# Performance work log

Measured on AMD Instinct MI355X. Metric: run time of the kernel, lower is better.

## Reference

```python
import jax, jax.numpy as jnp
from jax import lax
import numpy as np

GAMMA = 0.05   # GaussianKernel gamma (partial(GaussianKernel, 0.05)); assumed default for conv2 as well
EPS = 1e-5     # BatchNorm eps
DN = ('NCHW', 'OIHW', 'NCHW')


def gaussian_conv(x, w, gamma):
    """KernelConv2d with RBF kernel: out[b,o,i,j] = exp(-gamma * ||patch - w[o]||^2).
    Uses ||x-w||^2 = ||x||^2 - 2 x.w + ||w||^2 to avoid materializing im2col patches."""
    cross = lax.conv_general_dilated(x, w, (1, 1), 'VALID', dimension_numbers=DN)
    ones = jnp.ones((1, x.shape[1]) + w.shape[2:], x.dtype)
    xsq = lax.conv_general_dilated(x * x, ones, (1, 1), 'VALID', dimension_numbers=DN)
    wsq = jnp.sum(w * w, axis=(1, 2, 3))[None, :, None, None]
    return jnp.exp(-gamma * (xsq - 2.0 * cross + wsq))


def max_pool2(x):
    return lax.reduce_window(x, -jnp.inf, lax.max, (1, 1, 2, 2), (1, 1, 2, 2), 'VALID')


def batchnorm(x, g, b, m, v):
    # eval-mode BN with running stats
    scale = (g / jnp.sqrt(v + EPS))[None, :, None, None]
    return (x - m[None, :, None, None]) * scale + b[None, :, None, None]


def setup_inputs() -> dict:
    key = jax.random.key(0)
    ks = jax.random.split(key, 8)
    B, C, H = 128, 3, 96
    fea1, fea2, k1, k2, lin1, ncls = 32, 64, 5, 5, 256, 10
    flat = fea2 * 21 * 21  # 96->92->46->42->21
    return {
        'x': jax.random.normal(ks[0], (B, C, H, H), jnp.float32),
        'w1': jax.random.normal(ks[1], (fea1, C, k1, k1), jnp.float32) * 0.05,
        'w2': jax.random.normal(ks[2], (fea2, fea1, k2, k2), jnp.float32) * 0.05,
        'bn1_g': jnp.ones((fea1,), jnp.float32),
        'bn1_b': jnp.zeros((fea1,), jnp.float32),
        'bn1_m': jnp.zeros((fea1,), jnp.float32),
        'bn1_v': jnp.ones((fea1,), jnp.float32),
        'bn2_g': jnp.ones((fea2,), jnp.float32),
        'bn2_b': jnp.zeros((fea2,), jnp.float32),
        'bn2_m': jnp.zeros((fea2,), jnp.float32),
        'bn2_v': jnp.ones((fea2,), jnp.float32),
        'fc1_w': jax.random.normal(ks[3], (lin1, flat), jnp.float32) * 0.02,
        'fc1_b': jnp.zeros((lin1,), jnp.float32),
        'fc2_w': jax.random.normal(ks[4], (ncls, lin1), jnp.float32) * 0.02,
        'fc2_b': jnp.zeros((ncls,), jnp.float32),
    }


def reference(x, w1, w2, bn1_g, bn1_b, bn1_m, bn1_v, bn2_g, bn2_b, bn2_m, bn2_v,
              fc1_w, fc1_b, fc2_w, fc2_b):
    h = jax.nn.relu(max_pool2(gaussian_conv(x, w1, GAMMA)))
    h = batchnorm(h, bn1_g, bn1_b, bn1_m, bn1_v)
    # eval mode: Dropout2d is identity
    h = jax.nn.relu(max_pool2(gaussian_conv(h, w2, GAMMA)))
    h = batchnorm(h, bn2_g, bn2_b, bn2_m, bn2_v)
    h = h.reshape(h.shape[0], -1)
    h = jax.nn.relu(h @ fc1_w.T + fc1_b)
    # eval mode: dropout is identity
    h = jax.nn.relu(h @ fc2_w.T + fc2_b)
    return jax.nn.log_softmax(h, axis=1)
```

## Files before the change

kernel.cpp:

```cpp
#include <hip/hip_runtime.h>
#include <math.h>

#define GAMMA 0.05f
#define EPSBN 1e-5f

#define B_   128
#define H0   96
#define O1   32
#define P1   46
#define O2   64
#define H2C  42
#define P2   21
#define FLAT (O2*P2*P2)
#define L1N  256
#define NCLS 10
#define XW   104

typedef __attribute__((ext_vector_type(8))) short bf16x8;
typedef __attribute__((ext_vector_type(4))) float f32x4;
typedef __attribute__((ext_vector_type(16))) float f32x16;

static __device__ __forceinline__ float bf2f(unsigned short h) {
    return __uint_as_float(((unsigned int)h) << 16);
}
static __device__ __forceinline__ unsigned short f2bf(float f) {
    unsigned int u = __float_as_uint(f);
    u = (u + 0x7FFFu + ((u >> 16) & 1u)) >> 16;
    return (unsigned short)u;
}

__global__ void k_wprep(const float* __restrict__ w1, const float* __restrict__ w2,
                        unsigned short* __restrict__ w2bf, unsigned short* __restrict__ w1p8,
                        float* __restrict__ wsq1, float* __restrict__ wsq2) {
    int pb = blockIdx.x;
    int tid = threadIdx.x;
    for (int i = pb * 256 + tid; i < 51200 + 7168; i += 64 * 256) {
        if (i < 51200) {
            int e = i & 7, o = (i >> 3) & 63, hi = (i >> 9) & 1, ks = (i >> 10) & 1, kp = i >> 11;
            int ch = ks * 16 + hi * 8 + e;
            w2bf[i] = f2bf(-2.f * w2[((size_t)o * 32 + ch) * 25 + kp]);
        } else {
            int j = i - 51200;
            int ch = j & 7, o = (j >> 3) & 31, t = j >> 8;
            float v = 0.f;
            if (t < 25) {
                if (ch < 3) v = -2.f * w1[(size_t)(o * 3 + ch) * 25 + t];
                else if (ch == 3) v = 1.f;
            }
            w1p8[j] = f2bf(v);
        }
    }
    if (pb == 0) {
        int lt = tid;
        if (lt < 32) {
            const float* p = w1 + lt * 75;
            float s = 0.f;
            for (int i = 0; i < 75; ++i) s += p[i] * p[i];
            wsq1[lt] = s;
        } else if (lt < 96) {
            const float* p = w2 + (size_t)(lt - 32) * 800;
            float s = 0.f;
            for (int i = 0; i < 800; ++i) s += p[i] * p[i];
            wsq2[lt - 32] = s;
        }
    }
}

__global__ __launch_bounds__(256) void k_conv1m(
    const float* __restrict__ x, const unsigned short* __restrict__ w1p8,
    const float* __restrict__ wsq1,
    const float* __restrict__ g, const float* __restrict__ bb_,
    const float* __restrict__ m, const float* __restrict__ v,
    unsigned short* __restrict__ h1t) {
    __shared__ unsigned short xt[1536 * 8];
    int b = blockIdx.y;
    int pi0 = blockIdx.x * 4;
    int tid = threadIdx.x;
    {
        const float* xb = x + (size_t)b * 3 * 9216;
        float va[6], vc[6], vd[6];
        int ok[6];
        #pragma unroll
        for (int it = 0; it < 6; ++it) {
            int c = tid + it * 256;
            int cs = c < 1352 ? c : 1351;
            int rr = cs / XW, cc2 = cs - rr * XW;
            int srow = 2 * pi0 + rr; if (srow > 95) srow = 95;
            ok[it] = (cc2 < 96);
            int off = srow * 96 + (cc2 < 96 ? cc2 : 95);
            va[it] = xb[off];
            vc[it] = xb[9216 + off];
            vd[it] = xb[18432 + off];
        }
        #pragma unroll
        for (int it = 0; it < 6; ++it) {
            int c = tid + it * 256;
            unsigned int p0 = 0, p1 = 0;
            if (ok[it]) {
                float a = va[it], cch = vc[it], dd = vd[it];
                float s = a * a + cch * cch + dd * dd;
                p0 = (unsigned)f2bf(a) | ((unsigned)f2bf(cch) << 16);
                p1 = (unsigned)f2bf(dd) | ((unsigned)f2bf(s) << 16);
            }
            uint4 pk; pk.x = p0; pk.y = p1; pk.z = 0; pk.w = 0;
            *(uint4*)(xt + (size_t)c * 8) = pk;
        }
    }
    __syncthreads();
    int w = tid >> 6, lane = tid & 63;
    int pi = pi0 + w;
    if (pi >= P1) return;
    int l15 = lane & 15, l4 = lane >> 4;

    bf16x8 Bf[7][2];
    int kio[7], kjo[7];
    #pragma unroll
    for (int mm = 0; mm < 7; ++mm) {
        int t = mm * 4 + l4;
        kio[mm] = t / 5; kjo[mm] = t - kio[mm] * 5;
        #pragma unroll
        for (int nt = 0; nt < 2; ++nt)
            Bf[mm][nt] = *(const bf16x8*)(w1p8 + ((size_t)t * 32 + nt * 16 + l15) * 8);
    }
    float wqa[2], sca[2], moa[2], boa[2];
    #pragma unroll
    for (int nt = 0; nt < 2; ++nt) {
        int o = nt * 16 + l15;
        wqa[nt] = wsq1[o];
        sca[nt] = g[o] * rsqrtf(v[o] + EPSBN);
        moa[nt] = m[o]; boa[nt] = bb_[o];
    }

    for (int s6 = 0; s6 < 6; ++s6) {
        int j0 = s6 * 16;
        f32x4 a0[2], a1[2];
        #pragma unroll
        for (int nt = 0; nt < 2; ++nt) {
            a0[nt] = (f32x4){0.f, 0.f, 0.f, 0.f};
            a1[nt] = (f32x4){0.f, 0.f, 0.f, 0.f};
        }
        {
            int ri = 2 * w;
            #pragma unroll
            for (int mm = 0; mm < 7; ++mm) {
                bf16x8 av = *(const bf16x8*)(xt + ((size_t)(ri + kio[mm]) * XW + j0 + l15 + kjo[mm]) * 8);
                a0[0] = __builtin_amdgcn_mfma_f32_16x16x32_bf16(av, Bf[mm][0], a0[0], 0, 0, 0);
                a0[1] = __builtin_amdgcn_mfma_f32_16x16x32_bf16(av, Bf[mm][1], a0[1], 0, 0, 0);
            }
            ri = 2 * w + 1;
            #pragma unroll
            for (int mm = 0; mm < 7; ++mm) {
                bf16x8 av = *(const bf16x8*)(xt + ((size_t)(ri + kio[mm]) * XW + j0 + l15 + kjo[mm]) * 8);
                a1[0] = __builtin_amdgcn_mfma_f32_16x16x32_bf16(av, Bf[mm][0], a1[0], 0, 0, 0);
                a1[1] = __builtin_amdgcn_mfma_f32_16x16x32_bf16(av, Bf[mm][1], a1[1], 0, 0, 0);
            }
        }
        #pragma unroll
        for (int q = 0; q < 2; ++q) {
            int pj = (j0 >> 1) + l4 * 2 + q;
            if (pj < P1) {
                #pragma unroll
                for (int nt = 0; nt < 2; ++nt) {
                    float d00 = a0[nt][2 * q]     + wqa[nt];
                    float d01 = a0[nt][2 * q + 1] + wqa[nt];
                    float d10 = a1[nt][2 * q]     + wqa[nt];
                    float d11 = a1[nt][2 * q + 1] + wqa[nt];
                    float dm = fminf(fminf(d00, d01), fminf(d10, d11));
                    float y = (__expf(-GAMMA * dm) - moa[nt]) * sca[nt] + boa[nt];
                    h1t[((size_t)b * 2116 + pi * P1 + pj) * 32 + nt * 16 + l15] = f2bf(y);
                }
            }
        }
    }
}

__global__ __launch_bounds__(256, 2) void k_conv2m(
    const unsigned short* __restrict__ h1t, const unsigned short* __restrict__ w2bf,
    const float* __restrict__ wsq2,
    const float* __restrict__ g2, const float* __restrict__ b2,
    const float* __restrict__ m2, const float* __restrict__ v2,
    unsigned short* __restrict__ h2t) {
    __shared__ unsigned short lds[2304 * 8];
    __shared__ float sst[12 * 46];
    __shared__ float rh[12 * 42];
    __shared__ float xq[8 * 42];
    int b = blockIdx.y;
    int bx = blockIdx.x;
    int rbase = 8 * bx;
    int tid = threadIdx.x;
    {
        uint4 tmp[9];
        #pragma unroll
        for (int it = 0; it < 9; ++it) {
            int c = tid + it * 256;
            int cs = c < 2208 ? c : 2207;
            int p = cs >> 2, s = cs & 3;
            int il = p / 46, jl = p - il * 46;
            int srow = rbase + il; if (srow > 45) srow = 45;
            int src_s = (s - il - jl) & 3;
            tmp[it] = *(const uint4*)(h1t + ((((size_t)b * 46 + srow) * 46 + jl) * 32) + src_s * 8);
        }
        #pragma unroll
        for (int it = 0; it < 9; ++it) {
            int c = tid + it * 256;
            *(uint4*)(lds + (size_t)c * 8) = tmp[it];
        }
    }
    __syncthreads();
    for (int p = tid; p < 552; p += 256) {
        float s2 = 0.f;
        #pragma unroll
        for (int sl = 0; sl < 4; ++sl) {
            bf16x8 v8 = *(const bf16x8*)(lds + (size_t)p * 32 + sl * 8);
            #pragma unroll
            for (int e = 0; e < 8; ++e) {
                float yv = bf2f((unsigned short)v8[e]);
                s2 = fmaf(yv, yv, s2);
            }
        }
        sst[p] = s2;
    }
    __syncthreads();
    for (int i = tid; i < 504; i += 256) {
        int r = i / 42, j = i - r * 42;
        const float* s = &sst[r * 46 + j];
        rh[i] = s[0] + s[1] + s[2] + s[3] + s[4];
    }
    __syncthreads();
    for (int i = tid; i < 336; i += 256) {
        const float* s = &rh[i];
        xq[i] = s[0] + s[42] + s[84] + s[126] + s[168];
    }
    __syncthreads();

    int lane = tid & 63, st = tid >> 6;
    int prow = 4 * bx + st;
    if (prow >= P2) return;
    int hi = lane >> 5;
    int ri = lane & 1;
    int cpos = (lane >> 1) & 15;
    int ol = lane & 31;

    float wqA[2], scA[2], moA[2], boA[2];
    #pragma unroll
    for (int nt = 0; nt < 2; ++nt) {
        int o = nt * 32 + ol;
        wqA[nt] = wsq2[o];
        scA[nt] = g2[o] * rsqrtf(v2[o] + EPSBN);
        moA[nt] = m2[o]; boA[nt] = b2[o];
    }

    f32x16 acc0[3], acc1[3];
    #pragma unroll
    for (int cg = 0; cg < 3; ++cg)
        #pragma unroll
        for (int e = 0; e < 16; ++e) { acc0[cg][e] = 0.f; acc1[cg][e] = 0.f; }

    #pragma unroll 1
    for (int ks = 0; ks < 2; ++ks) {
        const unsigned short* wb0 = w2bf + (((size_t)ks * 2 + hi) * 64 + ol) * 8;
        const unsigned short* wb1 = wb0 + 32 * 8;
        int sB = 2 * ks + hi;
        #pragma unroll 1
        for (int ki = 0; ki < 5; ++ki) {
            bf16x8 B0[5], B1[5];
            #pragma unroll
            for (int kj = 0; kj < 5; ++kj) {
                B0[kj] = *(const bf16x8*)(wb0 + (size_t)(ki * 5 + kj) * 2048);
                B1[kj] = *(const bf16x8*)(wb1 + (size_t)(ki * 5 + kj) * 2048);
            }
            int il = 2 * st + ri + ki;
            int base = il * 46;
            int sI = sB + il;
            #pragma unroll
            for (int cg = 0; cg < 3; ++cg) {
                #pragma unroll
                for (int kj = 0; kj < 5; ++kj) {
                    int jl = cg * 16 + cpos + kj; if (jl > 45) jl = 45;
                    int slot = (sI + jl) & 3;
                    bf16x8 av = *(const bf16x8*)(lds + (base + jl) * 32 + slot * 8);
                    acc0[cg] = __builtin_amdgcn_mfma_f32_32x32x16_bf16(av, B0[kj], acc0[cg], 0, 0, 0);
                    acc1[cg] = __builtin_amdgcn_mfma_f32_32x32x16_bf16(av, B1[kj], acc1[cg], 0, 0, 0);
                }
            }
        }
    }
    size_t bb = (size_t)b * FLAT;
    int lr = 2 * st;
    #pragma unroll
    for (int cg = 0; cg < 3; ++cg) {
        int j0 = cg * 16;
        #pragma unroll
        for (int q = 0; q < 4; ++q) {
            int wdw = 2 * q + hi;
            int pcol = cg * 8 + wdw;
            if (pcol < P2) {
                int jc = j0 + 2 * wdw;
                float x00 = xq[lr * 42 + jc],       x01 = xq[lr * 42 + jc + 1];
                float x10 = xq[(lr + 1) * 42 + jc], x11 = xq[(lr + 1) * 42 + jc + 1];
                int pp = prow * 21 + pcol;
                {
                    float d0 = x00 + acc0[cg][4 * q + 0] + wqA[0];
                    float d1 = x10 + acc0[cg][4 * q + 1] + wqA[0];
                    float d2 = x01 + acc0[cg][4 * q + 2] + wqA[0];
                    float d3 = x11 + acc0[cg][4 * q + 3] + wqA[0];
                    float dm = fminf(fminf(d0, d1), fminf(d2, d3));
                    float y = (__expf(-GAMMA * dm) - moA[0]) * scA[0] + boA[0];
                    h2t[bb + (size_t)ol * 441 + pp] = f2bf(y);
                }
                {
                    float d0 = x00 + acc1[cg][4 * q + 0] + wqA[1];
                    float d1 = x10 + acc1[cg][4 * q + 1] + wqA[1];
                    float d2 = x01 + acc1[cg][4 * q + 2] + wqA[1];
                    float d3 = x11 + acc1[cg][4 * q + 3] + wqA[1];
                    float dm = fminf(fminf(d0, d1), fminf(d2, d3));
                    float y = (__expf(-GAMMA * dm) - moA[1]) * scA[1] + boA[1];
                    h2t[bb + (size_t)(32 + ol) * 441 + pp] = f2bf(y);
                }
            }
        }
    }
}

__global__ __launch_bounds__(256) void k_fc1m(const unsigned short* __restrict__ A,
                                              const float* __restrict__ W,
                                              float* __restrict__ part) {
    __shared__ unsigned short Ws[64][456];
    int s = blockIdx.x;
    int nb = blockIdx.y;
    int n0 = nb * 64;
    int k0 = s * 448;
    int tid = threadIdx.x;
    for (int i = tid; i < 64 * 112; i += 256) {
        int n = i / 112, j = i - n * 112;
        float4 v = *(const float4*)(W + (size_t)(n0 + n) * FLAT + k0 + j * 4);
        unsigned int lo = (unsigned)f2bf(v.x) | ((unsigned)f2bf(v.y) << 16);
        unsigned int hi2 = (unsigned)f2bf(v.z) | ((unsigned)f2bf(v.w) << 16);
        uint2 pk; pk.x = lo; pk.y = hi2;
        *(uint2*)(&Ws[n][j * 4]) = pk;
    }
    __syncthreads();
    int lane = tid & 63, w = tid >> 6;
    int l15 = lane & 15, l4 = lane >> 4;
    const unsigned short* ap = A + (size_t)l15 * FLAT + k0 + l4 * 8;
    f32x4 acc[8];
    #pragma unroll
    for (int mf = 0; mf < 8; ++mf) acc[mf] = (f32x4){0.f, 0.f, 0.f, 0.f};
    #pragma unroll 2
    for (int kc = 0; kc < 14; ++kc) {
        bf16x8 Bf = *(const bf16x8*)(&Ws[w * 16 + l15][kc * 32 + l4 * 8]);
        #pragma unroll
        for (int mf = 0; mf < 8; ++mf) {
            bf16x8 Af = *(const bf16x8*)(ap + (size_t)mf * 16 * FLAT + kc * 32);
            acc[mf] = __builtin_amdgcn_mfma_f32_16x16x32_bf16(Af, Bf, acc[mf], 0, 0, 0);
        }
    }
    float* pp = part + (size_t)s * B_ * L1N;
    #pragma unroll
    for (int mf = 0; mf < 8; ++mf)
        #pragma unroll
        for (int r = 0; r < 4; ++r)
            pp[(size_t)(mf * 16 + l4 * 4 + r) * L1N + n0 + w * 16 + l15] = acc[mf][r];
}

__global__ void k_fc1red(const float* __restrict__ part, const float* __restrict__ bias,
                         float* __restrict__ fc1o) {
    int idx = blockIdx.x * blockDim.x + threadIdx.x;
    if (idx >= B_ * L1N) return;
    int o = idx & (L1N - 1);
    float s = 0.f;
    for (int ks = 0; ks < 63; ++ks) s += part[(size_t)ks * B_ * L1N + idx];
    fc1o[idx] = fmaxf(s + bias[o], 0.f);
}

__global__ void k_fc2(const float* __restrict__ a, const float* __restrict__ w,
                      const float* __restrict__ bias, float* __restrict__ out) {
    int b = blockIdx.x;
    int lane = threadIdx.x;
    __shared__ float z[NCLS];
    for (int j = 0; j < NCLS; ++j) {
        float p = 0.f;
        for (int k = lane; k < L1N; k += 64)
            p = fmaf(a[(size_t)b * L1N + k], w[(size_t)j * L1N + k], p);
        #pragma unroll
        for (int off = 32; off; off >>= 1) p += __shfl_down(p, off, 64);
        if (lane == 0) z[j] = fmaxf(p + bias[j], 0.f);
    }
    __syncthreads();
    if (lane == 0) {
        float mx = -1e30f;
        for (int j = 0; j < NCLS; ++j) mx = fmaxf(mx, z[j]);
        float s = 0.f;
        for (int j = 0; j < NCLS; ++j) s += expf(z[j] - mx);
        float l = logf(s);
        for (int j = 0; j < NCLS; ++j) out[(size_t)b * NCLS + j] = z[j] - mx - l;
    }
}

extern "C" void kernel_launch(void* const* d_in, const int* in_sizes, int n_in,
                              void* d_out, int out_size, void* d_ws, size_t ws_size,
                              hipStream_t stream) {
    const float* x    = (const float*)d_in[0];
    const float* w1   = (const float*)d_in[1];
    const float* w2   = (const float*)d_in[2];
    const float* bn1g = (const float*)d_in[3];
    const float* bn1b = (const float*)d_in[4];
    const float* bn1m = (const float*)d_in[5];
    const float* bn1v = (const float*)d_in[6];
    const float* bn2g = (const float*)d_in[7];
    const float* bn2b = (const float*)d_in[8];
    const float* bn2m = (const float*)d_in[9];
    const float* bn2v = (const float*)d_in[10];
    const float* fc1w = (const float*)d_in[11];
    const float* fc1b = (const float*)d_in[12];
    const float* fc2w = (const float*)d_in[13];
    const float* fc2b = (const float*)d_in[14];
    float* out = (float*)d_out;

    char* wsb = (char*)d_ws;
    unsigned short* h1t = (unsigned short*)wsb;  wsb += (size_t)B_ * 2116 * 32 * 2;
    unsigned short* h2t = (unsigned short*)wsb;  wsb += (size_t)B_ * FLAT * 2;
    float* part  = (float*)wsb;                  wsb += (size_t)63 * B_ * L1N * 4;
    float* fc1o  = (float*)wsb;                  wsb += (size_t)B_ * L1N * 4;
    unsigned short* w2bf = (unsigned short*)wsb; wsb += (size_t)51200 * 2;
    unsigned short* w1p8 = (unsigned short*)wsb; wsb += (size_t)28 * 32 * 8 * 2;
    float* wsq1 = (float*)wsb;                   wsb += 32 * 4;
    float* wsq2 = (float*)wsb;                   wsb += 64 * 4;

    k_wprep<<<64, 256, 0, stream>>>(w1, w2, w2bf, w1p8, wsq1, wsq2);
    k_conv1m<<<dim3(12, B_), 256, 0, stream>>>(
        x, w1p8, wsq1, bn1g, bn1b, bn1m, bn1v, h1t);
    k_conv2m<<<dim3(6, B_), 256, 0, stream>>>(
        h1t, w2bf, wsq2, bn2g, bn2b, bn2m, bn2v, h2t);
    k_fc1m<<<dim3(63, 4), 256, 0, stream>>>(h2t, fc1w, part);
    k_fc1red<<<(B_ * L1N + 255) / 256, 256, 0, stream>>>(part, fc1b, fc1o);
    k_fc2<<<B_, 64, 0, stream>>>(fc1o, fc2w, fc2b, out);
}
```

Baseline: 118.5 us.

## Pack two conv1 taps per MFMA k-group to drop zero padding

Conv1 previously padded each input pixel to 8 bf16 values (4 useful: 3 channels plus the squared norm), which wasted half of each MFMA K dimension. The input tile is now stored with 4 values per pixel, and each MFMA operand is built from two 8-byte LDS reads covering two different taps. This cuts the MFMAs per output row from 14 to 8 and halves the conv1 LDS footprint. In exchange it doubles the number of smaller LDS reads and reorders the packed weights to match the new tap pairing.

Result: no change. 116.7 us (-1.5%).

```diff
diff --git a/kernel.cpp b/kernel.cpp
--- a/kernel.cpp
+++ b/kernel.cpp
@@ -30,24 +30,26 @@
 }
 
 __global__ void k_wprep(const float* __restrict__ w1, const float* __restrict__ w2,
-                        unsigned short* __restrict__ w2bf, unsigned short* __restrict__ w1p8,
+                        unsigned short* __restrict__ w2bf, unsigned short* __restrict__ w1q,
                         float* __restrict__ wsq1, float* __restrict__ wsq2) {
     int pb = blockIdx.x;
     int tid = threadIdx.x;
-    for (int i = pb * 256 + tid; i < 51200 + 7168; i += 64 * 256) {
+    for (int i = pb * 256 + tid; i < 51200 + 4096; i += 64 * 256) {
         if (i < 51200) {
             int e = i & 7, o = (i >> 3) & 63, hi = (i >> 9) & 1, ks = (i >> 10) & 1, kp = i >> 11;
             int ch = ks * 16 + hi * 8 + e;
             w2bf[i] = f2bf(-2.f * w2[((size_t)o * 32 + ch) * 25 + kp]);
         } else {
             int j = i - 51200;
-            int ch = j & 7, o = (j >> 3) & 31, t = j >> 8;
+            int e = j & 7, o = (j >> 3) & 31, s = j >> 8;
+            int tap = (s >> 2) * 8 + 2 * (s & 3) + (e >> 2);
+            int ch = e & 3;
             float v = 0.f;
-            if (t < 25) {
-                if (ch < 3) v = -2.f * w1[(size_t)(o * 3 + ch) * 25 + t];
-                else if (ch == 3) v = 1.f;
-            }
-            w1p8[j] = f2bf(v);
+            if (tap < 25) {
+                if (ch < 3) v = -2.f * w1[(size_t)(o * 3 + ch) * 25 + tap];
+                else v = 1.f;
+            }
+            w1q[j] = f2bf(v);
         }
     }
     if (pb == 0) {
@@ -67,12 +69,12 @@
 }
 
 __global__ __launch_bounds__(256) void k_conv1m(
-    const float* __restrict__ x, const unsigned short* __restrict__ w1p8,
+    const float* __restrict__ x, const unsigned short* __restrict__ w1q,
     const float* __restrict__ wsq1,
     const float* __restrict__ g, const float* __restrict__ bb_,
     const float* __restrict__ m, const float* __restrict__ v,
     unsigned short* __restrict__ h1t) {
-    __shared__ unsigned short xt[1536 * 8];
+    __shared__ unsigned short xt4[1536 * 4];
     int b = blockIdx.y;
     int pi0 = blockIdx.x * 4;
     int tid = threadIdx.x;
@@ -102,8 +104,8 @@
                 p0 = (unsigned)f2bf(a) | ((unsigned)f2bf(cch) << 16);
                 p1 = (unsigned)f2bf(dd) | ((unsigned)f2bf(s) << 16);
             }
-            uint4 pk; pk.x = p0; pk.y = p1; pk.z = 0; pk.w = 0;
-            *(uint4*)(xt + (size_t)c * 8) = pk;
+            uint2 pk; pk.x = p0; pk.y = p1;
+            *(uint2*)(xt4 + (size_t)c * 4) = pk;
         }
     }
     __syncthreads();
@@ -112,16 +114,21 @@
     if (pi >= P1) return;
     int l15 = lane & 15, l4 = lane >> 4;
 
-    bf16x8 Bf[7][2];
-    int kio[7], kjo[7];
-    #pragma unroll
-    for (int mm = 0; mm < 7; ++mm) {
-        int t = mm * 4 + l4;
-        kio[mm] = t / 5; kjo[mm] = t - kio[mm] * 5;
+    int kiA[4], kjA[4], kiB[4], kjB[4];
+    #pragma unroll
+    for (int mm = 0; mm < 4; ++mm) {
+        int tA = mm * 8 + 2 * l4;
+        int tB = tA + 1;
+        kiA[mm] = (tA < 25) ? tA / 5 : 4;  kjA[mm] = (tA < 25) ? tA % 5 : 4;
+        kiB[mm] = (tB < 25) ? tB / 5 : 4;  kjB[mm] = (tB < 25) ? tB % 5 : 4;
+    }
+    bf16x8 Bq[4][2];
+    #pragma unroll
+    for (int mm = 0; mm < 4; ++mm)
         #pragma unroll
         for (int nt = 0; nt < 2; ++nt)
-            Bf[mm][nt] = *(const bf16x8*)(w1p8 + ((size_t)t * 32 + nt * 16 + l15) * 8);
-    }
+            Bq[mm][nt] = *(const bf16x8*)(w1q + (((size_t)(mm * 4 + l4)) * 32 + nt * 16 + l15) * 8);
+
     float wqa[2], sca[2], moa[2], boa[2];
     #pragma unroll
     for (int nt = 0; nt < 2; ++nt) {
@@ -140,19 +147,21 @@
             a1[nt] = (f32x4){0.f, 0.f, 0.f, 0.f};
         }
         {
-            int ri = 2 * w;
+            int r0 = 2 * w, r1 = 2 * w + 1;
             #pragma unroll
-            for (int mm = 0; mm < 7; ++mm) {
-                bf16x8 av = *(const bf16x8*)(xt + ((size_t)(ri + kio[mm]) * XW + j0 + l15 + kjo[mm]) * 8);
-                a0[0] = __builtin_amdgcn_mfma_f32_16x16x32_bf16(av, Bf[mm][0], a0[0], 0, 0, 0);
-                a0[1] = __builtin_amdgcn_mfma_f32_16x16x32_bf16(av, Bf[mm][1], a0[1], 0, 0, 0);
-            }
-            ri = 2 * w + 1;
-            #pragma unroll
-            for (int mm = 0; mm < 7; ++mm) {
-                bf16x8 av = *(const bf16x8*)(xt + ((size_t)(ri + kio[mm]) * XW + j0 + l15 + kjo[mm]) * 8);
-                a1[0] = __builtin_amdgcn_mfma_f32_16x16x32_bf16(av, Bf[mm][0], a1[0], 0, 0, 0);
-                a1[1] = __builtin_amdgcn_mfma_f32_16x16x32_bf16(av, Bf[mm][1], a1[1], 0, 0, 0);
+            for (int mm = 0; mm < 4; ++mm) {
+                uint2 lo0 = *(const uint2*)(xt4 + ((size_t)(r0 + kiA[mm]) * XW + j0 + l15 + kjA[mm]) * 4);
+                uint2 hi0 = *(const uint2*)(xt4 + ((size_t)(r0 + kiB[mm]) * XW + j0 + l15 + kjB[mm]) * 4);
+                uint2 lo1 = *(const uint2*)(xt4 + ((size_t)(r1 + kiA[mm]) * XW + j0 + l15 + kjA[mm]) * 4);
+                uint2 hi1 = *(const uint2*)(xt4 + ((size_t)(r1 + kiB[mm]) * XW + j0 + l15 + kjB[mm]) * 4);
+                uint4 u0; u0.x = lo0.x; u0.y = lo0.y; u0.z = hi0.x; u0.w = hi0.y;
+                uint4 u1; u1.x = lo1.x; u1.y = lo1.y; u1.z = hi1.x; u1.w = hi1.y;
+                bf16x8 av0 = *(bf16x8*)&u0;
+                bf16x8 av1 = *(bf16x8*)&u1;
+                a0[0] = __builtin_amdgcn_mfma_f32_16x16x32_bf16(av0, Bq[mm][0], a0[0], 0, 0, 0);
+                a0[1] = __builtin_amdgcn_mfma_f32_16x16x32_bf16(av0, Bq[mm][1], a0[1], 0, 0, 0);
+                a1[0] = __builtin_amdgcn_mfma_f32_16x16x32_bf16(av1, Bq[mm][0], a1[0], 0, 0, 0);
+                a1[1] = __builtin_amdgcn_mfma_f32_16x16x32_bf16(av1, Bq[mm][1], a1[1], 0, 0, 0);
             }
         }
         #pragma unroll
@@ -423,13 +432,13 @@
     float* part  = (float*)wsb;                  wsb += (size_t)63 * B_ * L1N * 4;
     float* fc1o  = (float*)wsb;                  wsb += (size_t)B_ * L1N * 4;
     unsigned short* w2bf = (unsigned short*)wsb; wsb += (size_t)51200 * 2;
-    unsigned short* w1p8 = (unsigned short*)wsb; wsb += (size_t)28 * 32 * 8 * 2;
+    unsigned short* w1q  = (unsigned short*)wsb; wsb += (size_t)4096 * 2;
     float* wsq1 = (float*)wsb;                   wsb += 32 * 4;
     float* wsq2 = (float*)wsb;                   wsb += 64 * 4;
 
-    k_wprep<<<64, 256, 0, stream>>>(w1, w2, w2bf, w1p8, wsq1, wsq2);
+    k_wprep<<<64, 256, 0, stream>>>(w1, w2, w2bf, w1q, wsq1, wsq2);
     k_conv1m<<<dim3(12, B_), 256, 0, stream>>>(
-        x, w1p8, wsq1, bn1g, bn1b, bn1m, bn1v, h1t);
+        x, w1q, wsq1, bn1g, bn1b, bn1m, bn1v, h1t);
     k_conv2m<<<dim3(6, B_), 256, 0, stream>>>(
         h1t, w2bf, wsq2, bn2g, bn2b, bn2m, bn2v, h2t);
     k_fc1m<<<dim3(63, 4), 256, 0, stream>>>(h2t, fc1w, part);
```
